# Optimization experiments

Hardware: AMD Instinct MI355X
Metric: run time of the kernel (lower is better)

## Reference

```python
import jax, jax.numpy as jnp
import numpy as np

DIM = 128
NUM_HEADS = 4
HEAD_DIM = DIM // NUM_HEADS
WS = 8            # window height/width
SHIFT = 4
N_CAND = 4        # candidates per spatial position
H_RES, W_RES = 64, 128
M = WS * WS       # tokens per window spatially
L = M * N_CAND    # window sequence length
NW = (H_RES // WS) * (W_RES // WS)
B = 1
B_ = NW * B
NEG_INF = -1e9  # finite stand-in for -inf; softmax result identical within fp tolerance


def _rel_position_index():
    ch = np.arange(WS); cw = np.arange(WS)
    coords = np.stack(np.meshgrid(ch, cw, indexing='ij')).reshape(2, -1)  # [2, M]
    rel = (coords[:, :, None] - coords[:, None, :]).transpose(1, 2, 0)    # [M, M, 2]
    rel = rel + np.array([WS - 1, WS - 1])
    rel[..., 0] *= 2 * WS - 1
    return rel.sum(-1).astype(np.int32)  # [M, M] in [0, (2WS-1)^2)


def _window_attn_mask():
    # block message passing between same spatial position's candidates (except self)
    idx = np.repeat(np.arange(M), N_CAND).astype(np.float64)  # [L]
    m = idx[:, None] - idx[None, :]
    mask = np.where(m == 0, NEG_INF, 0.0)
    mask[np.arange(L), np.arange(L)] = 0.0
    return mask  # [L, L]


def _shift_window_attn_mask():
    img = np.zeros((H_RES, W_RES))
    cnt = 0
    for hs in (slice(0, -WS), slice(-WS, -SHIFT), slice(-SHIFT, None)):
        for ws in (slice(0, -WS), slice(-WS, -SHIFT), slice(-SHIFT, None)):
            img[hs, ws] = cnt
            cnt += 1
    mw = img.reshape(H_RES // WS, WS, W_RES // WS, WS).transpose(0, 2, 1, 3).reshape(-1, M)  # [nW, M]
    am = mw[:, None, :] - mw[:, :, None]           # [nW, M, M]
    am = np.where(am != 0, NEG_INF, 0.0)
    am = np.repeat(np.repeat(am, N_CAND, axis=1), N_CAND, axis=2)  # [nW, L, L]
    return am + _window_attn_mask()[None]


def setup_inputs() -> dict:
    key = jax.random.key(0)
    ks = jax.random.split(key, 6)
    x = jax.random.normal(ks[0], (B_, L, DIM), dtype=jnp.float32)
    qkv_w = jax.random.normal(ks[1], (3 * DIM, DIM), dtype=jnp.float32) * 0.02
    qkv_b = jnp.zeros((3 * DIM,), dtype=jnp.float32)
    rpe_table = jax.random.normal(ks[2], ((2 * WS - 1) ** 2, 3 * DIM), dtype=jnp.float32) * 0.02
    proj_w = jax.random.normal(ks[3], (DIM, DIM), dtype=jnp.float32) * 0.02
    proj_b = jnp.zeros((DIM,), dtype=jnp.float32)
    attn_mask = jnp.asarray(_shift_window_attn_mask(), dtype=jnp.float32)
    rel_idx = jnp.asarray(_rel_position_index())
    return {"x": x, "qkv_w": qkv_w, "qkv_b": qkv_b, "rpe_table": rpe_table,
            "proj_w": proj_w, "proj_b": proj_b, "attn_mask": attn_mask, "rel_idx": rel_idx}


def reference(x, qkv_w, qkv_b, rpe_table, proj_w, proj_b, attn_mask, rel_idx):
    b_, l, _ = x.shape
    h, hd = NUM_HEADS, HEAD_DIM
    scale = hd ** -0.5
    # QKV projection -> [B_, h, L, hd] each
    qkv = (x @ qkv_w.T + qkv_b).reshape(b_, l, 3, h, hd).transpose(2, 0, 3, 1, 4)
    q, k, v = qkv[0], qkv[1], qkv[2]
    # relative-position encodings gathered per (i, j) pair, expanded over candidates
    m = rel_idx.shape[0]
    n = l // m
    rpe = rpe_table[rel_idx.reshape(-1)].reshape(m, m, h, 3 * hd)
    rpe = jnp.repeat(jnp.repeat(rpe, n, axis=0), n, axis=1)  # [L, L, h, 3*hd]
    q_rpe, k_rpe, v_rpe = jnp.split(rpe, 3, axis=-1)
    q = q * scale
    q_rpe = q_rpe * scale
    qk = jnp.einsum('bhic,bhjc->bhij', q, k)
    qr = jnp.einsum('bhic,ijhc->bhij', q, k_rpe)
    kr = jnp.einsum('bhjc,ijhc->bhij', k, q_rpe)
    attn = qk + qr + kr  # [B_, h, L, L]
    nw = attn_mask.shape[0]
    attn = attn.reshape(b_ // nw, nw, h, l, l) + attn_mask[None, :, None]
    attn = attn.reshape(b_, h, l, l)
    attn = jax.nn.softmax(attn.astype(jnp.float32), axis=-1).astype(x.dtype)
    out = jnp.einsum('bhij,bhjc->bhic', attn, v) + jnp.einsum('bhij,ijhc->bhic', attn, v_rpe)
    out = out.transpose(0, 2, 1, 3).reshape(b_, l, DIM)
    return out @ proj_w.T + proj_b
```

## Files before the change

### kernel.cpp

```cpp
#include <hip/hip_runtime.h>
#include <math.h>

constexpr int HD    = 32;
constexpr int LW    = 256;
constexpr int NWIN  = 128;
constexpr int ROWS  = NWIN * LW;
constexpr int QKVC  = 384;
constexpr float SCALE = 0.17677669529663687f;

__device__ inline float dot4(const float4 a, const float4 b) {
  return a.x * b.x + a.y * b.y + a.z * b.z + a.w * b.w;
}

__global__ __launch_bounds__(256) void rpe_gather_kernel(
    const float* __restrict__ tab, const int* __restrict__ rel_idx,
    float* __restrict__ out)
{
  int gid = blockIdx.x * 256 + threadIdx.x;
  int s   = gid % 96;
  int hp  = gid / 96;
  int p   = hp & 4095;
  int h   = hp >> 12;
  float v = tab[(size_t)rel_idx[p] * 384 + h * 96 + s];
  if (s < 32) v *= SCALE;
  out[gid] = v;
}

template <int N, int K>
__global__ __launch_bounds__(256) void gemm_nt_bias_v3(
    const float* __restrict__ A, const float* __restrict__ W,
    const float* __restrict__ bias, float* __restrict__ C)
{
  constexpr int BK  = 8;
  constexpr int NS  = K / BK;
  constexpr int LDP = 144;
  __shared__ float As[2][BK][LDP];
  __shared__ float Ws[2][BK][LDP];

  const int tid  = threadIdx.x;
  const int tx   = tid & 15;
  const int ty   = tid >> 4;
  const int srow = tid >> 1;
  const int skk  = (tid & 1) << 2;
  const int sphys = srow + ((srow >> 5) << 2);

  const float* Ag = A + ((size_t)blockIdx.x * 128 + srow) * K + skk;
  const float* Wg = W + ((size_t)blockIdx.y * 128 + srow) * K + skk;

  float4 ra = *(const float4*)(Ag);
  float4 rw = *(const float4*)(Wg);
  As[0][skk + 0][sphys] = ra.x; As[0][skk + 1][sphys] = ra.y;
  As[0][skk + 2][sphys] = ra.z; As[0][skk + 3][sphys] = ra.w;
  Ws[0][skk + 0][sphys] = rw.x; Ws[0][skk + 1][sphys] = rw.y;
  Ws[0][skk + 2][sphys] = rw.z; Ws[0][skk + 3][sphys] = rw.w;
  __syncthreads();

  const int mA = ty * 8; const int pA = mA + ((mA >> 5) << 2);
  const int mB = tx * 8; const int pB = mB + ((mB >> 5) << 2);

  float acc[8][8] = {};

  for (int s = 0; s < NS; ++s) {
    const int cur = s & 1;
    if (s + 1 < NS) {
      const int k0 = (s + 1) * BK;
      ra = *(const float4*)(Ag + k0);
      rw = *(const float4*)(Wg + k0);
    }
#pragma unroll
    for (int k = 0; k < BK; ++k) {
      float4 a0 = *(const float4*)&As[cur][k][pA];
      float4 a1 = *(const float4*)&As[cur][k][pA + 4];
      float4 b0 = *(const float4*)&Ws[cur][k][pB];
      float4 b1 = *(const float4*)&Ws[cur][k][pB + 4];
      float av[8] = {a0.x, a0.y, a0.z, a0.w, a1.x, a1.y, a1.z, a1.w};
      float bv[8] = {b0.x, b0.y, b0.z, b0.w, b1.x, b1.y, b1.z, b1.w};
#pragma unroll
      for (int i = 0; i < 8; ++i)
#pragma unroll
        for (int j = 0; j < 8; ++j)
          acc[i][j] += av[i] * bv[j];
    }
    if (s + 1 < NS) {
      const int nxt = (s + 1) & 1;
      As[nxt][skk + 0][sphys] = ra.x; As[nxt][skk + 1][sphys] = ra.y;
      As[nxt][skk + 2][sphys] = ra.z; As[nxt][skk + 3][sphys] = ra.w;
      Ws[nxt][skk + 0][sphys] = rw.x; Ws[nxt][skk + 1][sphys] = rw.y;
      Ws[nxt][skk + 2][sphys] = rw.z; Ws[nxt][skk + 3][sphys] = rw.w;
      __syncthreads();
    }
  }

  const int crow = blockIdx.x * 128 + ty * 8;
  const int ccol = blockIdx.y * 128 + tx * 8;
  float4 bb0 = *(const float4*)(bias + ccol);
  float4 bb1 = *(const float4*)(bias + ccol + 4);
#pragma unroll
  for (int i = 0; i < 8; ++i) {
    float4 r0, r1;
    r0.x = acc[i][0] + bb0.x; r0.y = acc[i][1] + bb0.y;
    r0.z = acc[i][2] + bb0.z; r0.w = acc[i][3] + bb0.w;
    r1.x = acc[i][4] + bb1.x; r1.y = acc[i][5] + bb1.y;
    r1.z = acc[i][6] + bb1.z; r1.w = acc[i][7] + bb1.w;
    *(float4*)(C + (size_t)(crow + i) * N + ccol)     = r0;
    *(float4*)(C + (size_t)(crow + i) * N + ccol + 4) = r1;
  }
}

__global__ __launch_bounds__(256) void attn_kernel(
    const float* __restrict__ qkv, const float* __restrict__ rpeg,
    const float* __restrict__ mask, float* __restrict__ out)
{
  constexpr int JT = 64;
  constexpr int NT = LW / JT;
  __shared__ float kvs[2][2 * JT * HD];
  const int b = blockIdx.x;
  const int h = blockIdx.y;
  const int tid = threadIdx.x;
  const size_t rowbase = (size_t)b * LW;

  auto ld_tile = [&](int t, float4* r) {
#pragma unroll
    for (int it = 0; it < 4; ++it) {
      const int f = tid + 256 * it;
      const int kv = f >> 9, rr = f & 511;
      const int j = rr >> 3, d4 = rr & 7;
      r[it] = *(const float4*)(qkv + (rowbase + t * JT + j) * QKVC +
                               128 + kv * 128 + h * HD + d4 * 4);
    }
  };
  auto st_tile = [&](int buf, const float4* r) {
#pragma unroll
    for (int it = 0; it < 4; ++it) {
      const int f = tid + 256 * it;
      *(float4*)(&kvs[buf][f * 4]) = r[it];
    }
  };

  float4 sreg[4];
  ld_tile(0, sreg);
  st_tile(0, sreg);

  float4 q[8];
  {
    const float4* qr = (const float4*)(qkv + (rowbase + tid) * QKVC + h * HD);
#pragma unroll
    for (int d = 0; d < 8; ++d) {
      float4 t = qr[d];
      q[d] = make_float4(t.x * SCALE, t.y * SCALE, t.z * SCALE, t.w * SCALE);
    }
  }
  const float4* rp4base =
      (const float4*)(rpeg + ((size_t)h * 4096 + (size_t)(tid >> 2) * 64) * 96);
  const float* mrow = mask + ((size_t)b * LW + tid) * LW;

  float4 acc[8];
#pragma unroll
  for (int d = 0; d < 8; ++d) acc[d] = make_float4(0.f, 0.f, 0.f, 0.f);
  float l_run = 0.f;

  for (int t = 0; t < NT; ++t) {
    if (t + 1 < NT) ld_tile(t + 1, sreg);
    __syncthreads();
    const float* Kt = kvs[t & 1];
    const float* Vt = kvs[t & 1] + JT * HD;

    for (int j4l = 0; j4l < JT / 4; ++j4l) {
      const int j4g = t * (JT / 4) + j4l;
      const float4* rp = rp4base + j4g * 24;
      float4 mv = *(const float4*)(mrow + j4g * 4);
      const float4* k0 = (const float4*)(Kt + (j4l * 4 + 0) * HD);
      const float4* k1 = (const float4*)(Kt + (j4l * 4 + 1) * HD);
      const float4* k2 = (const float4*)(Kt + (j4l * 4 + 2) * HD);
      const float4* k3 = (const float4*)(Kt + (j4l * 4 + 3) * HD);
      float c0 = 0.f;
      float s0 = mv.x, s1 = mv.y, s2 = mv.z, s3 = mv.w;
#pragma unroll
      for (int d = 0; d < 8; ++d) {
        float4 sq = rp[d];
        float4 kr = rp[8 + d];
        float4 uq = make_float4(q[d].x + sq.x, q[d].y + sq.y,
                                q[d].z + sq.z, q[d].w + sq.w);
        c0 += dot4(q[d], kr);
        s0 += dot4(uq, k0[d]);
        s1 += dot4(uq, k1[d]);
        s2 += dot4(uq, k2[d]);
        s3 += dot4(uq, k3[d]);
      }
      float p0 = __expf(s0 + c0), p1 = __expf(s1 + c0);
      float p2 = __expf(s2 + c0), p3 = __expf(s3 + c0);
      float pool = (p0 + p1) + (p2 + p3);
      l_run += pool;
      const float4* v0 = (const float4*)(Vt + (j4l * 4 + 0) * HD);
      const float4* v1 = (const float4*)(Vt + (j4l * 4 + 1) * HD);
      const float4* v2 = (const float4*)(Vt + (j4l * 4 + 2) * HD);
      const float4* v3 = (const float4*)(Vt + (j4l * 4 + 3) * HD);
#pragma unroll
      for (int d = 0; d < 8; ++d) {
        float4 vr = rp[16 + d];
        float4 a = acc[d];
        a.x += p0 * v0[d].x + p1 * v1[d].x + p2 * v2[d].x + p3 * v3[d].x + pool * vr.x;
        a.y += p0 * v0[d].y + p1 * v1[d].y + p2 * v2[d].y + p3 * v3[d].y + pool * vr.y;
        a.z += p0 * v0[d].z + p1 * v1[d].z + p2 * v2[d].z + p3 * v3[d].z + pool * vr.z;
        a.w += p0 * v0[d].w + p1 * v1[d].w + p2 * v2[d].w + p3 * v3[d].w + pool * vr.w;
        acc[d] = a;
      }
    }
    if (t + 1 < NT) st_tile((t + 1) & 1, sreg);
  }

  float inv = 1.f / l_run;
  float4* orow = (float4*)(out + (rowbase + tid) * (4 * HD) + h * HD);
#pragma unroll
  for (int d = 0; d < 8; ++d)
    orow[d] = make_float4(acc[d].x * inv, acc[d].y * inv,
                          acc[d].z * inv, acc[d].w * inv);
}

extern "C" void kernel_launch(void* const* d_in, const int* in_sizes, int n_in,
                              void* d_out, int out_size, void* d_ws, size_t ws_size,
                              hipStream_t stream) {
  (void)in_sizes; (void)n_in; (void)out_size; (void)ws_size;
  const float* x         = (const float*)d_in[0];
  const float* qkv_w     = (const float*)d_in[1];
  const float* qkv_b     = (const float*)d_in[2];
  const float* rpe_table = (const float*)d_in[3];
  const float* proj_w    = (const float*)d_in[4];
  const float* proj_b    = (const float*)d_in[5];
  const float* attn_mask = (const float*)d_in[6];
  const int*   rel_idx   = (const int*)d_in[7];
  float* out = (float*)d_out;

  float* qkvbuf = (float*)d_ws;
  float* rpeg   = qkvbuf + (size_t)ROWS * QKVC;
  float* attnb  = rpeg + (size_t)4 * 4096 * 96;

  hipLaunchKernelGGL(rpe_gather_kernel, dim3(6144), dim3(256), 0, stream,
                     rpe_table, rel_idx, rpeg);
  hipLaunchKernelGGL((gemm_nt_bias_v3<QKVC, 128>), dim3(ROWS / 128, QKVC / 128),
                     dim3(256), 0, stream, x, qkv_w, qkv_b, qkvbuf);
  hipLaunchKernelGGL(attn_kernel, dim3(NWIN, 4), dim3(256), 0, stream,
                     qkvbuf, rpeg, attn_mask, attnb);
  hipLaunchKernelGGL((gemm_nt_bias_v3<128, 128>), dim3(ROWS / 128, 1),
                     dim3(256), 0, stream, attnb, proj_w, proj_b, out);
}
```

Baseline: 369.4 us.

## Split attention key range across two thread halves and load full K/V into LDS

The attention kernel now runs 512 threads per block, with two threads per query row that each cover half of the key positions. Partial accumulators and row sums are combined through shared memory at the end. The full K/V window (64 KB) is loaded into LDS up front instead of being double-buffered in 64-key tiles. This doubles the number of waves working on each query row, which should hide the latency of the rpe and mask global loads and help fill the 512-block grid. In exchange it uses more LDS per block, which may limit occupancy, and adds a reduction step.

```diff
diff --git a/kernel.cpp b/kernel.cpp
--- a/kernel.cpp
+++ b/kernel.cpp
@@ -107,114 +107,116 @@
   }
 }
 
-__global__ __launch_bounds__(256) void attn_kernel(
+__global__ __launch_bounds__(512) void attn_kernel(
     const float* __restrict__ qkv, const float* __restrict__ rpeg,
     const float* __restrict__ mask, float* __restrict__ out)
 {
-  constexpr int JT = 64;
-  constexpr int NT = LW / JT;
-  __shared__ float kvs[2][2 * JT * HD];
+  __shared__ float kvs[2 * LW * HD];
   const int b = blockIdx.x;
   const int h = blockIdx.y;
   const int tid = threadIdx.x;
+  const int row = tid & 255;
+  const int jh  = tid >> 8;
   const size_t rowbase = (size_t)b * LW;
 
-  auto ld_tile = [&](int t, float4* r) {
-#pragma unroll
-    for (int it = 0; it < 4; ++it) {
-      const int f = tid + 256 * it;
-      const int kv = f >> 9, rr = f & 511;
-      const int j = rr >> 3, d4 = rr & 7;
-      r[it] = *(const float4*)(qkv + (rowbase + t * JT + j) * QKVC +
-                               128 + kv * 128 + h * HD + d4 * 4);
-    }
-  };
-  auto st_tile = [&](int buf, const float4* r) {
-#pragma unroll
-    for (int it = 0; it < 4; ++it) {
-      const int f = tid + 256 * it;
-      *(float4*)(&kvs[buf][f * 4]) = r[it];
-    }
-  };
-
-  float4 sreg[4];
-  ld_tile(0, sreg);
-  st_tile(0, sreg);
+#pragma unroll
+  for (int it = 0; it < 8; ++it) {
+    const int f  = tid + 512 * it;
+    const int kv = f >> 11;
+    const int rr = f & 2047;
+    const int j  = rr >> 3, d4 = rr & 7;
+    *(float4*)(&kvs[f * 4]) =
+        *(const float4*)(qkv + (rowbase + j) * QKVC + 128 + kv * 128 +
+                         h * HD + d4 * 4);
+  }
 
   float4 q[8];
   {
-    const float4* qr = (const float4*)(qkv + (rowbase + tid) * QKVC + h * HD);
+    const float4* qr = (const float4*)(qkv + (rowbase + row) * QKVC + h * HD);
 #pragma unroll
     for (int d = 0; d < 8; ++d) {
       float4 t = qr[d];
       q[d] = make_float4(t.x * SCALE, t.y * SCALE, t.z * SCALE, t.w * SCALE);
     }
   }
+  __syncthreads();
+
   const float4* rp4base =
-      (const float4*)(rpeg + ((size_t)h * 4096 + (size_t)(tid >> 2) * 64) * 96);
-  const float* mrow = mask + ((size_t)b * LW + tid) * LW;
+      (const float4*)(rpeg + ((size_t)h * 4096 + (size_t)(row >> 2) * 64) * 96);
+  const float* mrow = mask + ((size_t)b * LW + row) * LW;
 
   float4 acc[8];
 #pragma unroll
   for (int d = 0; d < 8; ++d) acc[d] = make_float4(0.f, 0.f, 0.f, 0.f);
   float l_run = 0.f;
 
-  for (int t = 0; t < NT; ++t) {
-    if (t + 1 < NT) ld_tile(t + 1, sreg);
-    __syncthreads();
-    const float* Kt = kvs[t & 1];
-    const float* Vt = kvs[t & 1] + JT * HD;
-
-    for (int j4l = 0; j4l < JT / 4; ++j4l) {
-      const int j4g = t * (JT / 4) + j4l;
-      const float4* rp = rp4base + j4g * 24;
-      float4 mv = *(const float4*)(mrow + j4g * 4);
-      const float4* k0 = (const float4*)(Kt + (j4l * 4 + 0) * HD);
-      const float4* k1 = (const float4*)(Kt + (j4l * 4 + 1) * HD);
-      const float4* k2 = (const float4*)(Kt + (j4l * 4 + 2) * HD);
-      const float4* k3 = (const float4*)(Kt + (j4l * 4 + 3) * HD);
-      float c0 = 0.f;
-      float s0 = mv.x, s1 = mv.y, s2 = mv.z, s3 = mv.w;
-#pragma unroll
-      for (int d = 0; d < 8; ++d) {
-        float4 sq = rp[d];
-        float4 kr = rp[8 + d];
-        float4 uq = make_float4(q[d].x + sq.x, q[d].y + sq.y,
-                                q[d].z + sq.z, q[d].w + sq.w);
-        c0 += dot4(q[d], kr);
-        s0 += dot4(uq, k0[d]);
-        s1 += dot4(uq, k1[d]);
-        s2 += dot4(uq, k2[d]);
-        s3 += dot4(uq, k3[d]);
-      }
-      float p0 = __expf(s0 + c0), p1 = __expf(s1 + c0);
-      float p2 = __expf(s2 + c0), p3 = __expf(s3 + c0);
-      float pool = (p0 + p1) + (p2 + p3);
-      l_run += pool;
-      const float4* v0 = (const float4*)(Vt + (j4l * 4 + 0) * HD);
-      const float4* v1 = (const float4*)(Vt + (j4l * 4 + 1) * HD);
-      const float4* v2 = (const float4*)(Vt + (j4l * 4 + 2) * HD);
-      const float4* v3 = (const float4*)(Vt + (j4l * 4 + 3) * HD);
-#pragma unroll
-      for (int d = 0; d < 8; ++d) {
-        float4 vr = rp[16 + d];
-        float4 a = acc[d];
-        a.x += p0 * v0[d].x + p1 * v1[d].x + p2 * v2[d].x + p3 * v3[d].x + pool * vr.x;
-        a.y += p0 * v0[d].y + p1 * v1[d].y + p2 * v2[d].y + p3 * v3[d].y + pool * vr.y;
-        a.z += p0 * v0[d].z + p1 * v1[d].z + p2 * v2[d].z + p3 * v3[d].z + pool * vr.z;
-        a.w += p0 * v0[d].w + p1 * v1[d].w + p2 * v2[d].w + p3 * v3[d].w + pool * vr.w;
-        acc[d] = a;
-      }
-    }
-    if (t + 1 < NT) st_tile((t + 1) & 1, sreg);
-  }
-
-  float inv = 1.f / l_run;
-  float4* orow = (float4*)(out + (rowbase + tid) * (4 * HD) + h * HD);
-#pragma unroll
-  for (int d = 0; d < 8; ++d)
-    orow[d] = make_float4(acc[d].x * inv, acc[d].y * inv,
-                          acc[d].z * inv, acc[d].w * inv);
+  for (int l = 0; l < 32; ++l) {
+    const int j4 = jh * 32 + l;
+    const float4* rp = rp4base + j4 * 24;
+    float4 mv = *(const float4*)(mrow + j4 * 4);
+    const float4* k0 = (const float4*)(&kvs[(j4 * 4 + 0) * HD]);
+    const float4* k1 = (const float4*)(&kvs[(j4 * 4 + 1) * HD]);
+    const float4* k2 = (const float4*)(&kvs[(j4 * 4 + 2) * HD]);
+    const float4* k3 = (const float4*)(&kvs[(j4 * 4 + 3) * HD]);
+    float c0 = 0.f;
+    float s0 = mv.x, s1 = mv.y, s2 = mv.z, s3 = mv.w;
+#pragma unroll
+    for (int d = 0; d < 8; ++d) {
+      float4 sq = rp[d];
+      float4 kr = rp[8 + d];
+      float4 uq = make_float4(q[d].x + sq.x, q[d].y + sq.y,
+                              q[d].z + sq.z, q[d].w + sq.w);
+      c0 += dot4(q[d], kr);
+      s0 += dot4(uq, k0[d]);
+      s1 += dot4(uq, k1[d]);
+      s2 += dot4(uq, k2[d]);
+      s3 += dot4(uq, k3[d]);
+    }
+    float p0 = __expf(s0 + c0), p1 = __expf(s1 + c0);
+    float p2 = __expf(s2 + c0), p3 = __expf(s3 + c0);
+    float pool = (p0 + p1) + (p2 + p3);
+    l_run += pool;
+    const float4* v0 = (const float4*)(&kvs[LW * HD + (j4 * 4 + 0) * HD]);
+    const float4* v1 = (const float4*)(&kvs[LW * HD + (j4 * 4 + 1) * HD]);
+    const float4* v2 = (const float4*)(&kvs[LW * HD + (j4 * 4 + 2) * HD]);
+    const float4* v3 = (const float4*)(&kvs[LW * HD + (j4 * 4 + 3) * HD]);
+#pragma unroll
+    for (int d = 0; d < 8; ++d) {
+      float4 vr = rp[16 + d];
+      float4 a = acc[d];
+      a.x += p0 * v0[d].x + p1 * v1[d].x + p2 * v2[d].x + p3 * v3[d].x + pool * vr.x;
+      a.y += p0 * v0[d].y + p1 * v1[d].y + p2 * v2[d].y + p3 * v3[d].y + pool * vr.y;
+      a.z += p0 * v0[d].z + p1 * v1[d].z + p2 * v2[d].z + p3 * v3[d].z + pool * vr.z;
+      a.w += p0 * v0[d].w + p1 * v1[d].w + p2 * v2[d].w + p3 * v3[d].w + pool * vr.w;
+      acc[d] = a;
+    }
+  }
+
+  __syncthreads();
+  if (jh == 1) {
+    float* dst = &kvs[row * 33];
+#pragma unroll
+    for (int d = 0; d < 8; ++d) {
+      dst[d * 4 + 0] = acc[d].x; dst[d * 4 + 1] = acc[d].y;
+      dst[d * 4 + 2] = acc[d].z; dst[d * 4 + 3] = acc[d].w;
+    }
+    dst[32] = l_run;
+  }
+  __syncthreads();
+  if (jh == 0) {
+    const float* src = &kvs[row * 33];
+    float inv = 1.f / (l_run + src[32]);
+    float4* orow = (float4*)(out + (rowbase + row) * (4 * HD) + h * HD);
+#pragma unroll
+    for (int d = 0; d < 8; ++d) {
+      float4 r;
+      r.x = (acc[d].x + src[d * 4 + 0]) * inv;
+      r.y = (acc[d].y + src[d * 4 + 1]) * inv;
+      r.z = (acc[d].z + src[d * 4 + 2]) * inv;
+      r.w = (acc[d].w + src[d * 4 + 3]) * inv;
+      orow[d] = r;
+    }
+  }
 }
 
 extern "C" void kernel_launch(void* const* d_in, const int* in_sizes, int n_in,
@@ -239,7 +241,7 @@
                      rpe_table, rel_idx, rpeg);
   hipLaunchKernelGGL((gemm_nt_bias_v3<QKVC, 128>), dim3(ROWS / 128, QKVC / 128),
                      dim3(256), 0, stream, x, qkv_w, qkv_b, qkvbuf);
-  hipLaunchKernelGGL(attn_kernel, dim3(NWIN, 4), dim3(256), 0, stream,
+  hipLaunchKernelGGL(attn_kernel, dim3(NWIN, 4), dim3(512), 0, stream,
                      qkvbuf, rpeg, attn_mask, attnb);
   hipLaunchKernelGGL((gemm_nt_bias_v3<128, 128>), dim3(ROWS / 128, 1),
                      dim3(256), 0, stream, attnb, proj_w, proj_b, out);
```

New measurement: 430.8 us. 1.17x slower.
